# Kernel optimization log

Hardware: AMD Instinct MI355X
Metric: run time of the kernel (lower is better)

## Reference

```python
import jax, jax.numpy as jnp
import numpy as np

B, LQ, LK = 4, 512, 512
QS, KS, H, DV = 512, 512, 256, 512


def setup_inputs() -> dict:
    key = jax.random.key(0)
    ks = jax.random.split(key, 9)
    s_q = 1.0 / np.sqrt(QS)
    s_k = 1.0 / np.sqrt(KS)
    s_v = 1.0 / np.sqrt(H)
    return {
        "query": jax.random.normal(ks[0], (B, LQ, QS), jnp.float32),
        "key": jax.random.normal(ks[1], (B, LK, KS), jnp.float32),
        "value": jax.random.normal(ks[2], (B, LK, DV), jnp.float32),
        "wq": jax.random.uniform(ks[3], (H, QS), jnp.float32, -s_q, s_q),
        "bq": jax.random.uniform(ks[4], (H,), jnp.float32, -s_q, s_q),
        "wk": jax.random.uniform(ks[5], (H, KS), jnp.float32, -s_k, s_k),
        "bk": jax.random.uniform(ks[6], (H,), jnp.float32, -s_k, s_k),
        "wv": jax.random.uniform(ks[7], (H,), jnp.float32, -s_v, s_v),
        "bv": jax.random.uniform(ks[8], (), jnp.float32, -s_v, s_v),
    }


def reference(query, key, value, wq, bq, wk, bk, wv, bv):
    # q: [B, Lq, H], k: [B, Lk, H]
    q = jnp.einsum('bqd,hd->bqh', query, wq) + bq
    k = jnp.einsum('bkd,hd->bkh', key, wk) + bk
    # broadcast add -> [B, Lq, Lk, H], tanh, project to scalar score
    feats = jnp.tanh(q[:, :, None, :] + k[:, None, :, :])
    scores = jnp.einsum('bqkh,h->bqk', feats, wv) + bv  # [B, Lq, Lk]
    attn = jax.nn.softmax(scores, axis=-1)
    # dropout p=0.0 (identity at inference)
    return jnp.einsum('bqk,bkd->bqd', attn, value)
```

## Files before the change

kernel.cpp:

```cpp
#include <hip/hip_runtime.h>

#define LOG2E 1.4426950408889634f

constexpr int Bb = 4, LQ = 512, LK = 512, QS = 512, H = 256, DV = 512;
constexpr int M = 2048;

constexpr size_t OFF_EQT = 0;
constexpr size_t OFF_EKT = 2u << 20;
constexpr size_t OFF_PQ  = 4u << 20;
constexpr size_t OFF_ROW = 6u << 20;
constexpr size_t OFF_VT  = 8u << 20;

using bf16x8 = __attribute__((ext_vector_type(8))) short;
using f32x4v = __attribute__((ext_vector_type(4))) float;

__device__ inline unsigned short f2bf(float x) {
    unsigned int u = __float_as_uint(x);
    u += 0x7FFFu + ((u >> 16) & 1u);
    return (unsigned short)(u >> 16);
}
__device__ inline unsigned int pk2(float lo, float hi) {
    unsigned int r;
    asm("v_cvt_pk_bf16_f32 %0, %1, %2" : "=v"(r) : "v"(lo), "v"(hi));
    return r;
}

__global__ __launch_bounds__(256) void proj_mfma(
    const float* __restrict__ query, const float* __restrict__ key,
    const float* __restrict__ wq, const float* __restrict__ wk,
    const float* __restrict__ bq, const float* __restrict__ bk,
    char* __restrict__ ws, float scale)
{
    const int z = blockIdx.z;
    const float* A    = z ? key : query;
    const float* W    = z ? wk : wq;
    const float* bias = z ? bk : bq;
    float* out = (float*)(ws + (z ? OFF_EKT : OFF_EQT));
    const float off = z ? 0.0f : 13.0f;

    __shared__ unsigned short Als[64][136];
    __shared__ unsigned short Wls[64][136];
    __shared__ float Ot[64][68];

    const int mb = blockIdx.x * 64, nb = blockIdx.y * 64;
    const int tid = threadIdx.x;
    const int wid = tid >> 6, lane = tid & 63;
    const int ml = lane & 15, quad = lane >> 4;

    f32x4v acc[4] = {{0,0,0,0},{0,0,0,0},{0,0,0,0},{0,0,0,0}};

    for (int kc = 0; kc < QS; kc += 128) {
        __syncthreads();
#pragma unroll
        for (int it = 0; it < 4; ++it) {
            int u = tid + it * 256;
            int row = u >> 4, c8 = (u & 15) * 8;
            float4 a0 = *(const float4*)(A + (size_t)(mb + row) * 512 + kc + c8);
            float4 a1 = *(const float4*)(A + (size_t)(mb + row) * 512 + kc + c8 + 4);
            uint4 pa = { pk2(a0.x, a0.y), pk2(a0.z, a0.w), pk2(a1.x, a1.y), pk2(a1.z, a1.w) };
            *(uint4*)&Als[row][c8] = pa;
            float4 w0 = *(const float4*)(W + (size_t)(nb + row) * 512 + kc + c8);
            float4 w1 = *(const float4*)(W + (size_t)(nb + row) * 512 + kc + c8 + 4);
            uint4 pw = { pk2(w0.x, w0.y), pk2(w0.z, w0.w), pk2(w1.x, w1.y), pk2(w1.z, w1.w) };
            *(uint4*)&Wls[row][c8] = pw;
        }
        __syncthreads();
#pragma unroll
        for (int s = 0; s < 4; ++s) {
            int k = s * 32 + quad * 8;
            bf16x8 af = *(const bf16x8*)&Als[wid * 16 + ml][k];
#pragma unroll
            for (int nt = 0; nt < 4; ++nt) {
                bf16x8 bfr = *(const bf16x8*)&Wls[nt * 16 + ml][k];
                acc[nt] = __builtin_amdgcn_mfma_f32_16x16x32_bf16(af, bfr, acc[nt], 0, 0, 0);
            }
        }
    }
    __syncthreads();
#pragma unroll
    for (int nt = 0; nt < 4; ++nt)
#pragma unroll
        for (int r = 0; r < 4; ++r)
            Ot[nt * 16 + ml][wid * 16 + quad * 4 + r] = acc[nt][r];
    __syncthreads();
    {
        int r0 = tid >> 2;
        int c0 = (tid & 3) * 16;
        float bs = bias[nb + r0];
#pragma unroll
        for (int g = 0; g < 4; ++g) {
            float4 v = *(const float4*)&Ot[r0][c0 + g * 4];
            float4 o;
            o.x = __builtin_amdgcn_exp2f(fminf(fmaxf(scale * (v.x + bs), -13.f), 13.f) - off);
            o.y = __builtin_amdgcn_exp2f(fminf(fmaxf(scale * (v.y + bs), -13.f), 13.f) - off);
            o.z = __builtin_amdgcn_exp2f(fminf(fmaxf(scale * (v.z + bs), -13.f), 13.f) - off);
            o.w = __builtin_amdgcn_exp2f(fminf(fmaxf(scale * (v.w + bs), -13.f), 13.f) - off);
            *(float4*)(out + (size_t)(nb + r0) * 2048 + mb + c0 + g * 4) = o;
        }
    }
}

__global__ __launch_bounds__(256) void vconv(
    const float* __restrict__ V, char* __restrict__ ws)
{
    unsigned short* VT = (unsigned short*)(ws + OFF_VT);
    __shared__ unsigned short T[64][72];
    const int b = blockIdx.z, k0 = blockIdx.x * 64, n0 = blockIdx.y * 64;
    const int tid = threadIdx.x;
    const float* Vb = V + (size_t)b * 512 * 512;
    const int r = tid >> 4, c = (tid & 15) * 4;
#pragma unroll
    for (int it = 0; it < 4; ++it) {
        int kr = r + it * 16;
        float4 v = *(const float4*)(Vb + (size_t)(k0 + kr) * 512 + n0 + c);
        T[c + 0][kr] = f2bf(v.x);
        T[c + 1][kr] = f2bf(v.y);
        T[c + 2][kr] = f2bf(v.z);
        T[c + 3][kr] = f2bf(v.w);
    }
    __syncthreads();
    const int rowO = tid >> 3, colO = (tid & 7) * 8;
#pragma unroll
    for (int it = 0; it < 2; ++it) {
        int n = rowO + it * 32;
        uint4 o = *(const uint4*)&T[n][colO];
        *(uint4*)(VT + ((size_t)b * 512 + n0 + n) * 512 + k0 + colO) = o;
    }
}

__global__ __launch_bounds__(512, 4) void score_kernel(
    const float* __restrict__ wvp, char* __restrict__ ws)
{
    const float* EqT = (const float*)(ws + OFF_EQT);
    const float* EkT = (const float*)(ws + OFF_EKT);
    unsigned short* Pq = (unsigned short*)(ws + OFF_PQ);
    float* rowpart = (float*)(ws + OFF_ROW);

    __shared__ float Qs[64][32];
    __shared__ float Ks[64][64];
    __shared__ float Wv2[H];
    __shared__ float redS[8][32];

    const int b  = blockIdx.z;
    const int qb = blockIdx.x * 32;
    const int kt = blockIdx.y;
    const int kb = kt * 64;
    const int tid = threadIdx.x;
    const int tx = tid & 15;
    const int ty = tid >> 4;
    const int w  = tid >> 6;
    const int lane = tid & 63;

    constexpr float S = 0.0001220703125f;
    if (tid < H) Wv2[tid] = wvp[tid] * (2.0f * LOG2E) * S;

    const int mq = b * LQ + qb;
    const int mk = b * LK + kb;

    float acc[2][2] = {};

    for (int h0 = 0; h0 < H; h0 += 64) {
        __syncthreads();
        {
            int hq = tid >> 3, cq = (tid & 7) * 4;
            *(float4*)&Qs[hq][cq] = *(const float4*)(EqT + (size_t)(h0 + hq) * M + mq + cq);
            int hk = tid >> 4, ck = (tid & 15) * 4;
            *(float4*)&Ks[hk][ck]      = *(const float4*)(EkT + (size_t)(h0 + hk) * M + mk + ck);
            *(float4*)&Ks[hk + 32][ck] = *(const float4*)(EkT + (size_t)(h0 + hk + 32) * M + mk + ck);
        }
        __syncthreads();
#pragma unroll 2
        for (int hh = 0; hh < 64; hh += 8) {
            float2 qv[8], kv[8];
#pragma unroll
            for (int u = 0; u < 8; ++u) qv[u] = *(const float2*)&Qs[hh + u][tx * 2];
#pragma unroll
            for (int u = 0; u < 8; ++u) kv[u] = *(const float2*)&Ks[hh + u][ty * 2];
            const float4 wA = *(const float4*)&Wv2[h0 + hh];
            const float4 wB = *(const float4*)&Wv2[h0 + hh + 4];
#pragma unroll
            for (int i = 0; i < 2; ++i)
#pragma unroll
                for (int j = 0; j < 2; ++j) {
                    float t[8];
#pragma unroll
                    for (int u = 0; u < 8; ++u)
                        t[u] = fmaf(i ? qv[u].y : qv[u].x, j ? kv[u].y : kv[u].x, S);
                    float t12 = t[0] * t[1], t34 = t[2] * t[3];
                    float n12 = fmaf(wA.x, t[1], wA.y * t[0]);
                    float n34 = fmaf(wA.z, t[3], wA.w * t[2]);
                    float numA = fmaf(n12, t34, n34 * t12);
                    float denA = t12 * t34;
                    float t56 = t[4] * t[5], t78 = t[6] * t[7];
                    float m12 = fmaf(wB.x, t[5], wB.y * t[4]);
                    float m34 = fmaf(wB.z, t[7], wB.w * t[6]);
                    float numB = fmaf(m12, t78, m34 * t56);
                    float denB = t56 * t78;
                    float NUMv = fmaf(numA, denB, numB * denA);
                    float DENv = denA * denB;
                    acc[i][j] = fmaf(NUMv, __builtin_amdgcn_rcpf(DENv), acc[i][j]);
                }
        }
    }

    float ps[2];
#pragma unroll
    for (int i = 0; i < 2; ++i) {
        int q = qb + tx * 2 + i;
        float p0 = __builtin_amdgcn_exp2f(-acc[i][0]);
        float p1 = __builtin_amdgcn_exp2f(-acc[i][1]);
        ps[i] = p0 + p1;
        *(unsigned int*)(Pq + ((size_t)(b * 512 + q) * 512 + kb + ty * 2)) = pk2(p0, p1);
    }
#pragma unroll
    for (int i = 0; i < 2; ++i) {
        ps[i] += __shfl_xor(ps[i], 16, 64);
        ps[i] += __shfl_xor(ps[i], 32, 64);
    }
    if (lane < 16) {
#pragma unroll
        for (int i = 0; i < 2; ++i) redS[w][tx * 2 + i] = ps[i];
    }
    __syncthreads();
    if (tid < 32) {
        float s = ((redS[0][tid] + redS[1][tid]) + (redS[2][tid] + redS[3][tid]))
                + ((redS[4][tid] + redS[5][tid]) + (redS[6][tid] + redS[7][tid]));
        rowpart[(size_t)kt * 2048 + b * 512 + qb + tid] = s;
    }
}

__global__ __launch_bounds__(512, 2) void av_mfma(
    const char* __restrict__ wsc, float* __restrict__ O)
{
    const unsigned short* Pq = (const unsigned short*)(wsc + OFF_PQ);
    const unsigned short* VT = (const unsigned short*)(wsc + OFF_VT);
    const float* rowpart = (const float*)(wsc + OFF_ROW);

    __shared__ unsigned short Pls[64][136];
    __shared__ unsigned short Vls[64][136];

    const int b = blockIdx.z, qb = blockIdx.x * 64, nb = blockIdx.y * 64;
    const int tid = threadIdx.x;
    const int wid = tid >> 6, lane = tid & 63;
    const int ml = lane & 15, quad = lane >> 4;
    const int ms = wid & 3, nh = wid >> 2;
    const unsigned short* Pb = Pq + (size_t)b * 512 * 512;
    const unsigned short* Vb = VT + (size_t)b * 512 * 512;

    f32x4v acc[2] = {{0,0,0,0},{0,0,0,0}};

    for (int kc = 0; kc < LK; kc += 128) {
        __syncthreads();
#pragma unroll
        for (int it = 0; it < 2; ++it) {
            int u = tid + it * 512;
            int row = u >> 4, c8 = (u & 15) * 8;
            *(uint4*)&Pls[row][c8] = *(const uint4*)(Pb + (size_t)(qb + row) * 512 + kc + c8);
            *(uint4*)&Vls[row][c8] = *(const uint4*)(Vb + (size_t)(nb + row) * 512 + kc + c8);
        }
        __syncthreads();
#pragma unroll
        for (int s = 0; s < 4; ++s) {
            int k = s * 32 + quad * 8;
            bf16x8 af = *(const bf16x8*)&Pls[ms * 16 + ml][k];
#pragma unroll
            for (int t = 0; t < 2; ++t) {
                bf16x8 bfr = *(const bf16x8*)&Vls[(nh * 2 + t) * 16 + ml][k];
                acc[t] = __builtin_amdgcn_mfma_f32_16x16x32_bf16(af, bfr, acc[t], 0, 0, 0);
            }
        }
    }

    float rr[4];
#pragma unroll
    for (int r = 0; r < 4; ++r) {
        int q = qb + ms * 16 + quad * 4 + r;
        float rs = 0.f;
#pragma unroll
        for (int t8 = 0; t8 < 8; ++t8) rs += rowpart[(size_t)t8 * 2048 + b * 512 + q];
        rr[r] = 1.0f / rs;
    }
#pragma unroll
    for (int t = 0; t < 2; ++t)
#pragma unroll
        for (int r = 0; r < 4; ++r) {
            int q = qb + ms * 16 + quad * 4 + r;
            O[((size_t)b * 512 + q) * 512 + nb + (nh * 2 + t) * 16 + ml] = acc[t][r] * rr[r];
        }
}

extern "C" void kernel_launch(void* const* d_in, const int* in_sizes, int n_in,
                              void* d_out, int out_size, void* d_ws, size_t ws_size,
                              hipStream_t stream) {
    const float* query = (const float*)d_in[0];
    const float* key   = (const float*)d_in[1];
    const float* value = (const float*)d_in[2];
    const float* wq    = (const float*)d_in[3];
    const float* bq    = (const float*)d_in[4];
    const float* wk    = (const float*)d_in[5];
    const float* bk    = (const float*)d_in[6];
    const float* wv    = (const float*)d_in[7];
    float* out = (float*)d_out;
    char* ws = (char*)d_ws;

    const float c2 = 2.0f * LOG2E;

    proj_mfma<<<dim3(32, 4, 2), 256, 0, stream>>>(query, key, wq, wk, bq, bk, ws, c2);
    vconv<<<dim3(8, 8, Bb), 256, 0, stream>>>(value, ws);
    score_kernel<<<dim3(16, 8, Bb), 512, 0, stream>>>(wv, ws);
    av_mfma<<<dim3(8, 8, Bb), 512, 0, stream>>>(ws, out);
}
```

Measured before the change: 118.7 us.

## Pre-convert projection inputs to bf16 and load MFMA fragments directly from global

Adds a preconv kernel that converts query/key/weights to bf16 in workspace and also performs the V transpose, replacing the separate vconv launch. proj_mfma and av_mfma drop their LDS staging and __syncthreads loops and instead read MFMA fragments straight from global memory, with 512 threads per block in the projection. This aims to cut LDS traffic and barriers and to halve projection input bytes. The cost is an extra pass over the inputs and strided, uncoalesced-per-lane global loads that depend on cache reuse.

```diff
diff --git a/kernel.cpp b/kernel.cpp
--- a/kernel.cpp
+++ b/kernel.cpp
@@ -10,6 +10,11 @@
 constexpr size_t OFF_PQ  = 4u << 20;
 constexpr size_t OFF_ROW = 6u << 20;
 constexpr size_t OFF_VT  = 8u << 20;
+constexpr size_t OFF_ABF = 10u << 20;
+constexpr size_t OFF_WBF = 14u << 20;
+
+constexpr int QN = 2048 * 512;
+constexpr int WN = 256 * 512;
 
 using bf16x8 = __attribute__((ext_vector_type(8))) short;
 using f32x4v = __attribute__((ext_vector_type(4))) float;
@@ -25,70 +30,111 @@
     return r;
 }
 
-__global__ __launch_bounds__(256) void proj_mfma(
+__global__ __launch_bounds__(256) void preconv(
     const float* __restrict__ query, const float* __restrict__ key,
     const float* __restrict__ wq, const float* __restrict__ wk,
+    const float* __restrict__ V, char* __restrict__ ws)
+{
+    const int tid = threadIdx.x;
+    if (blockIdx.z == 0) {
+        int base = (blockIdx.x * 256 + tid) * 16;
+        const float* src;
+        unsigned short* dst;
+        if (base < QN) {
+            src = query + base;
+            dst = (unsigned short*)(ws + OFF_ABF) + base;
+        } else if (base < 2 * QN) {
+            src = key + (base - QN);
+            dst = (unsigned short*)(ws + OFF_ABF) + base;
+        } else if (base < 2 * QN + WN) {
+            src = wq + (base - 2 * QN);
+            dst = (unsigned short*)(ws + OFF_WBF) + (base - 2 * QN);
+        } else {
+            src = wk + (base - 2 * QN - WN);
+            dst = (unsigned short*)(ws + OFF_WBF) + (base - 2 * QN);
+        }
+        float4 a = *(const float4*)(src);
+        float4 b = *(const float4*)(src + 4);
+        float4 c = *(const float4*)(src + 8);
+        float4 d = *(const float4*)(src + 12);
+        uint4 o0 = { pk2(a.x, a.y), pk2(a.z, a.w), pk2(b.x, b.y), pk2(b.z, b.w) };
+        uint4 o1 = { pk2(c.x, c.y), pk2(c.z, c.w), pk2(d.x, d.y), pk2(d.z, d.w) };
+        *(uint4*)(dst)     = o0;
+        *(uint4*)(dst + 8) = o1;
+    } else {
+        if (blockIdx.x >= 256) return;
+        unsigned short* VT = (unsigned short*)(ws + OFF_VT);
+        __shared__ unsigned short T[64][72];
+        const int id = blockIdx.x;
+        const int b = id >> 6, k0 = (id & 7) * 64, n0 = ((id >> 3) & 7) * 64;
+        const float* Vb = V + (size_t)b * 512 * 512;
+        const int r = tid >> 4, c = (tid & 15) * 4;
+#pragma unroll
+        for (int it = 0; it < 4; ++it) {
+            int kr = r + it * 16;
+            float4 v = *(const float4*)(Vb + (size_t)(k0 + kr) * 512 + n0 + c);
+            T[c + 0][kr] = f2bf(v.x);
+            T[c + 1][kr] = f2bf(v.y);
+            T[c + 2][kr] = f2bf(v.z);
+            T[c + 3][kr] = f2bf(v.w);
+        }
+        __syncthreads();
+        const int rowO = tid >> 3, colO = (tid & 7) * 8;
+#pragma unroll
+        for (int it = 0; it < 2; ++it) {
+            int n = rowO + it * 32;
+            uint4 o = *(const uint4*)&T[n][colO];
+            *(uint4*)(VT + ((size_t)b * 512 + n0 + n) * 512 + k0 + colO) = o;
+        }
+    }
+}
+
+__global__ __launch_bounds__(512, 2) void proj_mfma(
     const float* __restrict__ bq, const float* __restrict__ bk,
     char* __restrict__ ws, float scale)
 {
     const int z = blockIdx.z;
-    const float* A    = z ? key : query;
-    const float* W    = z ? wk : wq;
+    const unsigned short* Abf = (const unsigned short*)(ws + OFF_ABF) + (size_t)z * QN;
+    const unsigned short* Wbf = (const unsigned short*)(ws + OFF_WBF) + (size_t)z * WN;
     const float* bias = z ? bk : bq;
     float* out = (float*)(ws + (z ? OFF_EKT : OFF_EQT));
     const float off = z ? 0.0f : 13.0f;
 
-    __shared__ unsigned short Als[64][136];
-    __shared__ unsigned short Wls[64][136];
     __shared__ float Ot[64][68];
 
     const int mb = blockIdx.x * 64, nb = blockIdx.y * 64;
     const int tid = threadIdx.x;
     const int wid = tid >> 6, lane = tid & 63;
     const int ml = lane & 15, quad = lane >> 4;
-
-    f32x4v acc[4] = {{0,0,0,0},{0,0,0,0},{0,0,0,0},{0,0,0,0}};
-
-    for (int kc = 0; kc < QS; kc += 128) {
-        __syncthreads();
-#pragma unroll
-        for (int it = 0; it < 4; ++it) {
-            int u = tid + it * 256;
-            int row = u >> 4, c8 = (u & 15) * 8;
-            float4 a0 = *(const float4*)(A + (size_t)(mb + row) * 512 + kc + c8);
-            float4 a1 = *(const float4*)(A + (size_t)(mb + row) * 512 + kc + c8 + 4);
-            uint4 pa = { pk2(a0.x, a0.y), pk2(a0.z, a0.w), pk2(a1.x, a1.y), pk2(a1.z, a1.w) };
-            *(uint4*)&Als[row][c8] = pa;
-            float4 w0 = *(const float4*)(W + (size_t)(nb + row) * 512 + kc + c8);
-            float4 w1 = *(const float4*)(W + (size_t)(nb + row) * 512 + kc + c8 + 4);
-            uint4 pw = { pk2(w0.x, w0.y), pk2(w0.z, w0.w), pk2(w1.x, w1.y), pk2(w1.z, w1.w) };
-            *(uint4*)&Wls[row][c8] = pw;
-        }
-        __syncthreads();
-#pragma unroll
-        for (int s = 0; s < 4; ++s) {
-            int k = s * 32 + quad * 8;
-            bf16x8 af = *(const bf16x8*)&Als[wid * 16 + ml][k];
-#pragma unroll
-            for (int nt = 0; nt < 4; ++nt) {
-                bf16x8 bfr = *(const bf16x8*)&Wls[nt * 16 + ml][k];
-                acc[nt] = __builtin_amdgcn_mfma_f32_16x16x32_bf16(af, bfr, acc[nt], 0, 0, 0);
-            }
-        }
-    }
+    const int ms = wid & 3, nh = wid >> 2;
+
+    const unsigned short* Ap  = Abf + (size_t)(mb + ms * 16 + ml) * 512 + quad * 8;
+    const unsigned short* Wp0 = Wbf + (size_t)(nb + (nh * 2 + 0) * 16 + ml) * 512 + quad * 8;
+    const unsigned short* Wp1 = Wbf + (size_t)(nb + (nh * 2 + 1) * 16 + ml) * 512 + quad * 8;
+
+    f32x4v acc0 = {0, 0, 0, 0}, acc1 = {0, 0, 0, 0};
+#pragma unroll
+    for (int kk = 0; kk < 16; ++kk) {
+        bf16x8 af = *(const bf16x8*)(Ap  + kk * 32);
+        bf16x8 b0 = *(const bf16x8*)(Wp0 + kk * 32);
+        bf16x8 b1 = *(const bf16x8*)(Wp1 + kk * 32);
+        acc0 = __builtin_amdgcn_mfma_f32_16x16x32_bf16(af, b0, acc0, 0, 0, 0);
+        acc1 = __builtin_amdgcn_mfma_f32_16x16x32_bf16(af, b1, acc1, 0, 0, 0);
+    }
+
     __syncthreads();
 #pragma unroll
-    for (int nt = 0; nt < 4; ++nt)
-#pragma unroll
-        for (int r = 0; r < 4; ++r)
-            Ot[nt * 16 + ml][wid * 16 + quad * 4 + r] = acc[nt][r];
+    for (int r = 0; r < 4; ++r) {
+        Ot[(nh * 2 + 0) * 16 + ml][ms * 16 + quad * 4 + r] = acc0[r];
+        Ot[(nh * 2 + 1) * 16 + ml][ms * 16 + quad * 4 + r] = acc1[r];
+    }
     __syncthreads();
     {
-        int r0 = tid >> 2;
-        int c0 = (tid & 3) * 16;
+        int r0 = tid >> 3;
+        int c0 = (tid & 7) * 8;
         float bs = bias[nb + r0];
 #pragma unroll
-        for (int g = 0; g < 4; ++g) {
+        for (int g = 0; g < 2; ++g) {
             float4 v = *(const float4*)&Ot[r0][c0 + g * 4];
             float4 o;
             o.x = __builtin_amdgcn_exp2f(fminf(fmaxf(scale * (v.x + bs), -13.f), 13.f) - off);
@@ -97,34 +143,6 @@
             o.w = __builtin_amdgcn_exp2f(fminf(fmaxf(scale * (v.w + bs), -13.f), 13.f) - off);
             *(float4*)(out + (size_t)(nb + r0) * 2048 + mb + c0 + g * 4) = o;
         }
-    }
-}
-
-__global__ __launch_bounds__(256) void vconv(
-    const float* __restrict__ V, char* __restrict__ ws)
-{
-    unsigned short* VT = (unsigned short*)(ws + OFF_VT);
-    __shared__ unsigned short T[64][72];
-    const int b = blockIdx.z, k0 = blockIdx.x * 64, n0 = blockIdx.y * 64;
-    const int tid = threadIdx.x;
-    const float* Vb = V + (size_t)b * 512 * 512;
-    const int r = tid >> 4, c = (tid & 15) * 4;
-#pragma unroll
-    for (int it = 0; it < 4; ++it) {
-        int kr = r + it * 16;
-        float4 v = *(const float4*)(Vb + (size_t)(k0 + kr) * 512 + n0 + c);
-        T[c + 0][kr] = f2bf(v.x);
-        T[c + 1][kr] = f2bf(v.y);
-        T[c + 2][kr] = f2bf(v.z);
-        T[c + 3][kr] = f2bf(v.w);
-    }
-    __syncthreads();
-    const int rowO = tid >> 3, colO = (tid & 7) * 8;
-#pragma unroll
-    for (int it = 0; it < 2; ++it) {
-        int n = rowO + it * 32;
-        uint4 o = *(const uint4*)&T[n][colO];
-        *(uint4*)(VT + ((size_t)b * 512 + n0 + n) * 512 + k0 + colO) = o;
     }
 }
 
@@ -236,39 +254,27 @@
     const unsigned short* VT = (const unsigned short*)(wsc + OFF_VT);
     const float* rowpart = (const float*)(wsc + OFF_ROW);
 
-    __shared__ unsigned short Pls[64][136];
-    __shared__ unsigned short Vls[64][136];
-
     const int b = blockIdx.z, qb = blockIdx.x * 64, nb = blockIdx.y * 64;
     const int tid = threadIdx.x;
     const int wid = tid >> 6, lane = tid & 63;
     const int ml = lane & 15, quad = lane >> 4;
     const int ms = wid & 3, nh = wid >> 2;
-    const unsigned short* Pb = Pq + (size_t)b * 512 * 512;
-    const unsigned short* Vb = VT + (size_t)b * 512 * 512;
-
-    f32x4v acc[2] = {{0,0,0,0},{0,0,0,0}};
-
-    for (int kc = 0; kc < LK; kc += 128) {
-        __syncthreads();
-#pragma unroll
-        for (int it = 0; it < 2; ++it) {
-            int u = tid + it * 512;
-            int row = u >> 4, c8 = (u & 15) * 8;
-            *(uint4*)&Pls[row][c8] = *(const uint4*)(Pb + (size_t)(qb + row) * 512 + kc + c8);
-            *(uint4*)&Vls[row][c8] = *(const uint4*)(Vb + (size_t)(nb + row) * 512 + kc + c8);
-        }
-        __syncthreads();
-#pragma unroll
-        for (int s = 0; s < 4; ++s) {
-            int k = s * 32 + quad * 8;
-            bf16x8 af = *(const bf16x8*)&Pls[ms * 16 + ml][k];
-#pragma unroll
-            for (int t = 0; t < 2; ++t) {
-                bf16x8 bfr = *(const bf16x8*)&Vls[(nh * 2 + t) * 16 + ml][k];
-                acc[t] = __builtin_amdgcn_mfma_f32_16x16x32_bf16(af, bfr, acc[t], 0, 0, 0);
-            }
-        }
+
+    const unsigned short* Pp  = Pq + (size_t)b * 512 * 512
+                              + (size_t)(qb + ms * 16 + ml) * 512 + quad * 8;
+    const unsigned short* Vp0 = VT + (size_t)b * 512 * 512
+                              + (size_t)(nb + (nh * 2 + 0) * 16 + ml) * 512 + quad * 8;
+    const unsigned short* Vp1 = VT + (size_t)b * 512 * 512
+                              + (size_t)(nb + (nh * 2 + 1) * 16 + ml) * 512 + quad * 8;
+
+    f32x4v acc0 = {0, 0, 0, 0}, acc1 = {0, 0, 0, 0};
+#pragma unroll
+    for (int kk = 0; kk < 16; ++kk) {
+        bf16x8 af = *(const bf16x8*)(Pp  + kk * 32);
+        bf16x8 b0 = *(const bf16x8*)(Vp0 + kk * 32);
+        bf16x8 b1 = *(const bf16x8*)(Vp1 + kk * 32);
+        acc0 = __builtin_amdgcn_mfma_f32_16x16x32_bf16(af, b0, acc0, 0, 0, 0);
+        acc1 = __builtin_amdgcn_mfma_f32_16x16x32_bf16(af, b1, acc1, 0, 0, 0);
     }
 
     float rr[4];
@@ -281,12 +287,11 @@
         rr[r] = 1.0f / rs;
     }
 #pragma unroll
-    for (int t = 0; t < 2; ++t)
-#pragma unroll
-        for (int r = 0; r < 4; ++r) {
-            int q = qb + ms * 16 + quad * 4 + r;
-            O[((size_t)b * 512 + q) * 512 + nb + (nh * 2 + t) * 16 + ml] = acc[t][r] * rr[r];
-        }
+    for (int r = 0; r < 4; ++r) {
+        int q = qb + ms * 16 + quad * 4 + r;
+        O[((size_t)b * 512 + q) * 512 + nb + (nh * 2 + 0) * 16 + ml] = acc0[r] * rr[r];
+        O[((size_t)b * 512 + q) * 512 + nb + (nh * 2 + 1) * 16 + ml] = acc1[r] * rr[r];
+    }
 }
 
 extern "C" void kernel_launch(void* const* d_in, const int* in_sizes, int n_in,
@@ -305,8 +310,8 @@
 
     const float c2 = 2.0f * LOG2E;
 
-    proj_mfma<<<dim3(32, 4, 2), 256, 0, stream>>>(query, key, wq, wk, bq, bk, ws, c2);
-    vconv<<<dim3(8, 8, Bb), 256, 0, stream>>>(value, ws);
+    preconv<<<dim3(576, 1, 2), 256, 0, stream>>>(query, key, wq, wk, value, ws);
+    proj_mfma<<<dim3(32, 4, 2), 512, 0, stream>>>(bq, bk, ws, c2);
     score_kernel<<<dim3(16, 8, Bb), 512, 0, stream>>>(wv, ws);
     av_mfma<<<dim3(8, 8, Bb), 512, 0, stream>>>(ws, out);
 }
```

Result: slower. 131.0 us (+10.4%).
